# Optimization experiments

Hardware: AMD Instinct MI355X
Metric: run time of the kernel (lower is better)

Reference implementation:

```python
import jax, jax.numpy as jnp
import numpy as np

N_LAYERS = 2
N_COEF = 5
IN_DIM = 256
LN_EPS = 1e-6  # flax LayerNorm default


def jacobi_design(x, a, n):
    """Jacobi polynomials P_0..P_{n-1}^{(a,a)}(x). x: [...], returns [..., n]."""
    Ps = [jnp.ones_like(x)]
    if n > 1:
        Ps.append((a + 1.0) * x)
    for k in range(2, n):
        t = 2.0 * k + 2.0 * a
        A = 2.0 * k * (k + 2.0 * a) * (t - 2.0)
        B = (t - 1.0) * t * (t - 2.0)
        C = 2.0 * (k + a - 1.0) ** 2 * t
        Ps.append((B * x * Ps[-1] - C * Ps[-2]) / A)
    return jnp.stack(Ps, axis=-1)


def setup_inputs() -> dict:
    key = jax.random.key(0)
    k1, k2 = jax.random.split(key)
    x = jax.random.normal(k1, (8192, IN_DIM), dtype=jnp.float32)
    coefs = jax.random.normal(k2, (N_LAYERS, IN_DIM, IN_DIM, N_COEF), dtype=jnp.float32) * 0.03
    alphas = jnp.zeros((N_LAYERS,), dtype=jnp.float32)      # alpha_arctanh init zeros
    ln_scale = jnp.ones((N_LAYERS, IN_DIM), dtype=jnp.float32)
    ln_bias = jnp.zeros((N_LAYERS, IN_DIM), dtype=jnp.float32)
    return {"x": x, "coefs": coefs, "alphas": alphas, "ln_scale": ln_scale, "ln_bias": ln_bias}


def reference(x, coefs, alphas, ln_scale, ln_bias):
    h = x  # [B, D]
    for l in range(N_LAYERS):
        # LayerNorm
        mu = jnp.mean(h, axis=-1, keepdims=True)
        var = jnp.mean(jnp.square(h - mu), axis=-1, keepdims=True)
        hn = (h - mu) * jax.lax.rsqrt(var + LN_EPS) * ln_scale[l] + ln_bias[l]
        # KANLayer: Jacobi design matrix on tanh-mapped input
        a = jnp.tanh(alphas[l])
        dm = jacobi_design(jnp.tanh(hn), a, N_COEF)  # [B, D, C]
        # resid_scale=0, spline_scale=1, dropout inactive -> y = mean_i einsum
        in_dim = hn.shape[-1]
        h = jnp.einsum('bic,ioc->bo', dm, coefs[l]) / in_dim  # [B, D]
    return h
```

## Files before the change

### kernel.cpp

```cpp
#include <hip/hip_runtime.h>

#define D 256
#define NCOEF 5
#define KD 1280
#define NB 8192
#define NKC 160
#define PANEL (NKC * 512)

#define SXX_STRIDE 264
#define SXX_ELEMS (32 * SXX_STRIDE)

typedef __bf16 bf16;
typedef bf16 bf16x8 __attribute__((ext_vector_type(8)));
typedef bf16 bf16x4 __attribute__((ext_vector_type(4)));
typedef float f32x4 __attribute__((ext_vector_type(4)));

__device__ __forceinline__ void glds16(const bf16* g, bf16* l) {
    __builtin_amdgcn_global_load_lds((const __attribute__((address_space(1))) void*)g,
                                     (__attribute__((address_space(3))) void*)l, 16, 0, 0);
}

__global__ __launch_bounds__(256) void pack_kernel(const float* __restrict__ coefs,
                                                   bf16* __restrict__ Wt) {
    __shared__ float t[64 * 65];
    int b = blockIdx.x;
    int l = b / 80, rem = b % 80;
    int c = rem / 16, tl = rem % 16;
    int i0 = (tl >> 2) * 64, o0 = (tl & 3) * 64;

    for (int j = threadIdx.x; j < 4096; j += 256) {
        int i = j >> 6, o = j & 63;
        t[i * 65 + o] = coefs[(((size_t)(l * 256 + i0 + i)) * 256 + (o0 + o)) * 5 + c];
    }
    __syncthreads();
    bf16* dst = Wt + (size_t)l * (4 * PANEL)
                   + ((size_t)(tl & 3) * NKC + (c * 256 + i0) / 8) * 512;
    for (int j = threadIdx.x; j < 4096; j += 256) {
        int il = j & 7, o = (j >> 3) & 63, ih = j >> 9;
        dst[j] = (bf16)t[(ih * 8 + il) * 65 + o];
    }
}

template <int PH>
__device__ __forceinline__ void gemm_half(f32x4 (&acc)[2][4], const bf16* __restrict__ Wp,
                                          const bf16* sxx, bf16* sW, int l,
                                          float a1, const float* rB, const float* rC) {
#pragma unroll
    for (int it = 0; it < 20; ++it) {
        if (it == 19) __builtin_amdgcn_s_waitcnt(0x0F70);
        else          __builtin_amdgcn_s_waitcnt(0x0F74);
        const bf16* sWb = sW + (it & 1) * 2048;

        bf16x8 bfr[4];
#pragma unroll
        for (int tn = 0; tn < 4; ++tn)
            bfr[tn] = *(const bf16x8*)(sWb + (l >> 4) * 512 + (16 * tn + (l & 15)) * 8);

        const int kbase = PH * 640 + it * 32;
        const int c = kbase >> 8;
        const int i0 = (kbase & 255) + (l >> 4) * 8;

        bf16x8 af[2];
#pragma unroll
        for (int tm = 0; tm < 2; ++tm) {
            if (c == 0) {
#pragma unroll
                for (int j = 0; j < 8; ++j) af[tm][j] = (bf16)1.0f;
            } else {
                bf16x8 xv = *(const bf16x8*)(sxx + (16 * tm + (l & 15)) * SXX_STRIDE + i0);
#pragma unroll
                for (int j = 0; j < 8; ++j) {
                    float x = (float)xv[j];
                    float P;
                    if (c == 1)      P = a1 * x;
                    else if (c == 2) { float P1 = a1 * x; P = rB[0] * x * P1 - rC[0]; }
                    else if (c == 3) { float P1 = a1 * x; float P2 = rB[0] * x * P1 - rC[0];
                                       P = rB[1] * x * P2 - rC[1] * P1; }
                    else             { float P1 = a1 * x; float P2 = rB[0] * x * P1 - rC[0];
                                       float P3 = rB[1] * x * P2 - rC[1] * P1;
                                       P = rB[2] * x * P3 - rC[2] * P2; }
                    af[tm][j] = (bf16)P;
                }
            }
        }

#pragma unroll
        for (int tm = 0; tm < 2; ++tm)
#pragma unroll
            for (int tn = 0; tn < 4; ++tn)
                acc[tm][tn] = __builtin_amdgcn_mfma_f32_16x16x32_bf16(
                    af[tm], bfr[tn], acc[tm][tn], 0, 0, 0);

        if (it < 18) {
            __builtin_amdgcn_s_waitcnt(0xC07F);
            __builtin_amdgcn_sched_barrier(0);
            bf16* dst = sW + (it & 1) * 2048;
            const int kc0 = PH * 80 + (it + 2) * 4;
#pragma unroll
            for (int t = 0; t < 4; ++t)
                glds16(Wp + (kc0 + t) * 512 + l * 8, dst + t * 512);
        }
    }
}

__global__ __launch_bounds__(256, 2) void layer_kernel(
    const float* __restrict__ h, const float* __restrict__ scale,
    const float* __restrict__ bias, const float* __restrict__ alpha_p,
    const bf16* __restrict__ Wl, float* __restrict__ out) {
    __shared__ __align__(16) bf16 smem[SXX_ELEMS + 4 * 4096];

    const int tid = threadIdx.x;
    const int l   = tid & 63;
    const int w   = tid >> 6;
    const int g   = w >> 1, p = w & 1;
    const int slab = blockIdx.x >> 1;
    const int ch   = blockIdx.x & 1;

    bf16* sxx = smem;
    bf16* sW  = smem + SXX_ELEMS + w * 4096;

    const float a  = tanhf(alpha_p[0]);
    const float a1 = a + 1.f;
    float rB[3], rC[3];
#pragma unroll
    for (int k = 2; k < NCOEF; k++) {
        float tk  = 2.f * k + 2.f * a;
        float iAk = 1.f / (2.f * k * (k + 2.f * a) * (tk - 2.f));
        rB[k - 2] = (tk - 1.f) * tk * (tk - 2.f) * iAk;
        rC[k - 2] = 2.f * (k + a - 1.f) * (k + a - 1.f) * tk * iAk;
    }

    float4 sc4 = ((const float4*)scale)[l];
    float4 bi4 = ((const float4*)bias)[l];
    float scv[4] = {sc4.x, sc4.y, sc4.z, sc4.w};
    float biv[4] = {bi4.x, bi4.y, bi4.z, bi4.w};

    const float* hrows = h + (size_t)slab * 32 * D;
#pragma unroll
    for (int rr = 0; rr < 8; ++rr) {
        int lr = w * 8 + rr;
        float4 v = ((const float4*)(hrows + lr * D))[l];
        float s  = v.x + v.y + v.z + v.w;
        float ss = v.x * v.x + v.y * v.y + v.z * v.z + v.w * v.w;
#pragma unroll
        for (int off = 32; off > 0; off >>= 1) {
            s  += __shfl_down(s, off);
            ss += __shfl_down(ss, off);
        }
        s  = __shfl(s, 0);
        ss = __shfl(ss, 0);
        float mu   = s * (1.f / D);
        float rstd = rsqrtf(ss * (1.f / D) - mu * mu + 1e-6f);
        float hv[4] = {v.x, v.y, v.z, v.w};
        bf16x4 o;
#pragma unroll
        for (int e = 0; e < 4; ++e)
            o[e] = (bf16)tanhf((hv[e] - mu) * rstd * scv[e] + biv[e]);
        *(bf16x4*)(sxx + lr * SXX_STRIDE + 4 * l) = o;
    }

    const bf16* Wp = Wl + (size_t)(ch * 2 + g) * PANEL;
#pragma unroll
    for (int it = 0; it < 2; ++it) {
        bf16* dst = sW + it * 2048;
        const int kc0 = p * 80 + it * 4;
#pragma unroll
        for (int t = 0; t < 4; ++t)
            glds16(Wp + (kc0 + t) * 512 + l * 8, dst + t * 512);
    }
    __syncthreads();

    f32x4 acc[2][4] = {};
    if (p == 0) gemm_half<0>(acc, Wp, sxx, sW, l, a1, rB, rC);
    else        gemm_half<1>(acc, Wp, sxx, sW, l, a1, rB, rC);

    f32x4* dump = (f32x4*)(smem + SXX_ELEMS) + w * 512;
#pragma unroll
    for (int tm = 0; tm < 2; ++tm)
#pragma unroll
        for (int tn = 0; tn < 4; ++tn)
            dump[(tm * 4 + tn) * 64 + l] = acc[tm][tn];
    __syncthreads();

    if (p == 0) {
        f32x4* mine = dump;
        f32x4* part = dump + 512;
#pragma unroll
        for (int tm = 0; tm < 2; ++tm)
#pragma unroll
            for (int tn = 0; tn < 4; ++tn) {
                f32x4 v = mine[(tm * 4 + tn) * 64 + l] + part[(tm * 4 + tn) * 64 + l];
                v *= (1.f / 256.f);
                int gr = slab * 32 + 16 * tm + (l >> 4) * 4;
                int gc = ch * 128 + g * 64 + 16 * tn + (l & 15);
#pragma unroll
                for (int r = 0; r < 4; ++r)
                    out[(size_t)(gr + r) * D + gc] = v[r];
            }
    }
}

extern "C" void kernel_launch(void* const* d_in, const int* in_sizes, int n_in,
                              void* d_out, int out_size, void* d_ws, size_t ws_size,
                              hipStream_t stream) {
    const float* x        = (const float*)d_in[0];
    const float* coefs    = (const float*)d_in[1];
    const float* alphas   = (const float*)d_in[2];
    const float* ln_scale = (const float*)d_in[3];
    const float* ln_bias  = (const float*)d_in[4];
    float* out = (float*)d_out;

    char* ws = (char*)d_ws;
    bf16*  Wt = (bf16*)ws;
    float* h1 = (float*)(ws + 1310720);

    pack_kernel<<<160, 256, 0, stream>>>(coefs, Wt);
    layer_kernel<<<512, 256, 0, stream>>>(x, ln_scale, ln_bias, alphas, Wt, h1);
    layer_kernel<<<512, 256, 0, stream>>>(h1, ln_scale + D, ln_bias + D, alphas + 1,
                                          Wt + (size_t)4 * PANEL, out);
}
```

Baseline: 110.1 us.

## Fold constant P0 term into per-output bias and shrink GEMM K to 1024

The P0 Jacobi term is constant 1, so its contribution becomes a precomputed per-output bias (the column sum of coefs[...,0]), computed in extra pack_kernel blocks and added in the epilogue. This cuts GEMM K from 1280 to 1024. The remaining planes are reordered so each wave's pair of K-steps shares one evaluation of the polynomial recurrence, with the second operand cached in registers. tanhf is replaced by an exp-based fast tanh, which has slightly different accuracy near zero.

```diff
diff --git a/kernel.cpp b/kernel.cpp
--- a/kernel.cpp
+++ b/kernel.cpp
@@ -1,10 +1,9 @@
 #include <hip/hip_runtime.h>
 
 #define D 256
-#define NCOEF 5
-#define KD 1280
 #define NB 8192
-#define NKC 160
+#define KP 1024
+#define NKC 128
 #define PANEL (NKC * 512)
 
 #define SXX_STRIDE 264
@@ -20,34 +19,60 @@
                                      (__attribute__((address_space(3))) void*)l, 16, 0, 0);
 }
 
+__device__ __forceinline__ float fast_tanh(float x) {
+    float e = __expf(2.f * x);
+    return 1.f - 2.f / (e + 1.f);
+}
+
 __global__ __launch_bounds__(256) void pack_kernel(const float* __restrict__ coefs,
-                                                   bf16* __restrict__ Wt) {
+                                                   bf16* __restrict__ Wt,
+                                                   float* __restrict__ beta) {
     __shared__ float t[64 * 65];
+    __shared__ float accs[4][64];
     int b = blockIdx.x;
-    int l = b / 80, rem = b % 80;
-    int c = rem / 16, tl = rem % 16;
-    int i0 = (tl >> 2) * 64, o0 = (tl & 3) * 64;
-
-    for (int j = threadIdx.x; j < 4096; j += 256) {
-        int i = j >> 6, o = j & 63;
-        t[i * 65 + o] = coefs[(((size_t)(l * 256 + i0 + i)) * 256 + (o0 + o)) * 5 + c];
-    }
-    __syncthreads();
-    bf16* dst = Wt + (size_t)l * (4 * PANEL)
-                   + ((size_t)(tl & 3) * NKC + (c * 256 + i0) / 8) * 512;
-    for (int j = threadIdx.x; j < 4096; j += 256) {
-        int il = j & 7, o = (j >> 3) & 63, ih = j >> 9;
-        dst[j] = (bf16)t[(ih * 8 + il) * 65 + o];
+    if (b < 128) {
+        int l = b >> 6, rem = b & 63;
+        int c = (rem >> 4) + 1, tl = rem & 15;
+        int plane = (c == 1) ? 0 : (c == 4) ? 1 : (c == 2) ? 2 : 3;
+        int i0 = (tl >> 2) * 64, o0 = (tl & 3) * 64;
+
+        for (int j = threadIdx.x; j < 4096; j += 256) {
+            int i = j >> 6, o = j & 63;
+            t[i * 65 + o] = coefs[(((size_t)(l * 256 + i0 + i)) * 256 + (o0 + o)) * 5 + c];
+        }
+        __syncthreads();
+        bf16* dst = Wt + (size_t)l * (4 * PANEL)
+                       + ((size_t)(tl & 3) * NKC + (plane * 256 + i0) / 8) * 512;
+        for (int j = threadIdx.x; j < 4096; j += 256) {
+            int il = j & 7, o = (j >> 3) & 63, ih = j >> 9;
+            dst[j] = (bf16)t[(ih * 8 + il) * 65 + o];
+        }
+    } else {
+        int lidx = b - 128;
+        int l = lidx >> 2, o0 = (lidx & 3) * 64;
+        int o = threadIdx.x & 63, ig = threadIdx.x >> 6;
+        float sum = 0.f;
+        for (int m = 0; m < 64; ++m) {
+            int i = ig * 64 + m;
+            sum += coefs[(((size_t)(l * 256 + i)) * 256 + (o0 + o)) * 5 + 0];
+        }
+        accs[ig][o] = sum;
+        __syncthreads();
+        if (threadIdx.x < 64)
+            beta[l * 256 + o0 + threadIdx.x] = accs[0][threadIdx.x] + accs[1][threadIdx.x]
+                                             + accs[2][threadIdx.x] + accs[3][threadIdx.x];
     }
 }
 
 template <int PH>
 __device__ __forceinline__ void gemm_half(f32x4 (&acc)[2][4], const bf16* __restrict__ Wp,
-                                          const bf16* sxx, bf16* sW, int l,
-                                          float a1, const float* rB, const float* rC) {
-#pragma unroll
-    for (int it = 0; it < 20; ++it) {
-        if (it == 19) __builtin_amdgcn_s_waitcnt(0x0F70);
+                                          const bf16* sxx, bf16* sW, int l, float a1,
+                                          float rB0, float rB1, float rB2,
+                                          float rC0, float rC1, float rC2) {
+    bf16x8 afn[2];
+#pragma unroll
+    for (int it = 0; it < 16; ++it) {
+        if (it == 15) __builtin_amdgcn_s_waitcnt(0x0F70);
         else          __builtin_amdgcn_s_waitcnt(0x0F74);
         const bf16* sWb = sW + (it & 1) * 2048;
 
@@ -56,32 +81,29 @@
         for (int tn = 0; tn < 4; ++tn)
             bfr[tn] = *(const bf16x8*)(sWb + (l >> 4) * 512 + (16 * tn + (l & 15)) * 8);
 
-        const int kbase = PH * 640 + it * 32;
-        const int c = kbase >> 8;
-        const int i0 = (kbase & 255) + (l >> 4) * 8;
-
         bf16x8 af[2];
-#pragma unroll
-        for (int tm = 0; tm < 2; ++tm) {
-            if (c == 0) {
-#pragma unroll
-                for (int j = 0; j < 8; ++j) af[tm][j] = (bf16)1.0f;
-            } else {
+        if ((it & 1) == 0) {
+            const int j  = it >> 1;
+            const int i0 = j * 32 + (l >> 4) * 8;
+#pragma unroll
+            for (int tm = 0; tm < 2; ++tm) {
                 bf16x8 xv = *(const bf16x8*)(sxx + (16 * tm + (l & 15)) * SXX_STRIDE + i0);
 #pragma unroll
-                for (int j = 0; j < 8; ++j) {
-                    float x = (float)xv[j];
-                    float P;
-                    if (c == 1)      P = a1 * x;
-                    else if (c == 2) { float P1 = a1 * x; P = rB[0] * x * P1 - rC[0]; }
-                    else if (c == 3) { float P1 = a1 * x; float P2 = rB[0] * x * P1 - rC[0];
-                                       P = rB[1] * x * P2 - rC[1] * P1; }
-                    else             { float P1 = a1 * x; float P2 = rB[0] * x * P1 - rC[0];
-                                       float P3 = rB[1] * x * P2 - rC[1] * P1;
-                                       P = rB[2] * x * P3 - rC[2] * P2; }
-                    af[tm][j] = (bf16)P;
+                for (int jj = 0; jj < 8; ++jj) {
+                    float x  = (float)xv[jj];
+                    float P1 = a1 * x;
+                    float P2 = rB0 * x * P1 - rC0;
+                    float P3 = rB1 * x * P2 - rC1 * P1;
+                    float PA, PB;
+                    if (PH == 0) { PA = P1; PB = rB2 * x * P3 - rC2 * P2; }
+                    else         { PA = P2; PB = P3; }
+                    af[tm][jj]  = (bf16)PA;
+                    afn[tm][jj] = (bf16)PB;
                 }
             }
+        } else {
+            af[0] = afn[0];
+            af[1] = afn[1];
         }
 
 #pragma unroll
@@ -91,14 +113,15 @@
                 acc[tm][tn] = __builtin_amdgcn_mfma_f32_16x16x32_bf16(
                     af[tm], bfr[tn], acc[tm][tn], 0, 0, 0);
 
-        if (it < 18) {
+        if (it < 14) {
             __builtin_amdgcn_s_waitcnt(0xC07F);
             __builtin_amdgcn_sched_barrier(0);
+            const int itp   = it + 2;
+            const int chunk = (PH * 2 + (itp & 1)) * 8 + (itp >> 1);
             bf16* dst = sW + (it & 1) * 2048;
-            const int kc0 = PH * 80 + (it + 2) * 4;
 #pragma unroll
             for (int t = 0; t < 4; ++t)
-                glds16(Wp + (kc0 + t) * 512 + l * 8, dst + t * 512);
+                glds16(Wp + chunk * 2048 + t * 512 + l * 8, dst + t * 512);
         }
     }
 }
@@ -106,7 +129,8 @@
 __global__ __launch_bounds__(256, 2) void layer_kernel(
     const float* __restrict__ h, const float* __restrict__ scale,
     const float* __restrict__ bias, const float* __restrict__ alpha_p,
-    const bf16* __restrict__ Wl, float* __restrict__ out) {
+    const bf16* __restrict__ Wl, const float* __restrict__ beta,
+    float* __restrict__ out) {
     __shared__ __align__(16) bf16 smem[SXX_ELEMS + 4 * 4096];
 
     const int tid = threadIdx.x;
@@ -123,7 +147,7 @@
     const float a1 = a + 1.f;
     float rB[3], rC[3];
 #pragma unroll
-    for (int k = 2; k < NCOEF; k++) {
+    for (int k = 2; k < 5; k++) {
         float tk  = 2.f * k + 2.f * a;
         float iAk = 1.f / (2.f * k * (k + 2.f * a) * (tk - 2.f));
         rB[k - 2] = (tk - 1.f) * tk * (tk - 2.f) * iAk;
@@ -155,24 +179,24 @@
         bf16x4 o;
 #pragma unroll
         for (int e = 0; e < 4; ++e)
-            o[e] = (bf16)tanhf((hv[e] - mu) * rstd * scv[e] + biv[e]);
+            o[e] = (bf16)fast_tanh((hv[e] - mu) * rstd * scv[e] + biv[e]);
         *(bf16x4*)(sxx + lr * SXX_STRIDE + 4 * l) = o;
     }
 
     const bf16* Wp = Wl + (size_t)(ch * 2 + g) * PANEL;
 #pragma unroll
-    for (int it = 0; it < 2; ++it) {
-        bf16* dst = sW + it * 2048;
-        const int kc0 = p * 80 + it * 4;
+    for (int itp = 0; itp < 2; ++itp) {
+        bf16* dst = sW + itp * 2048;
+        const int chunk = (p * 2 + itp) * 8;
 #pragma unroll
         for (int t = 0; t < 4; ++t)
-            glds16(Wp + (kc0 + t) * 512 + l * 8, dst + t * 512);
+            glds16(Wp + chunk * 2048 + t * 512 + l * 8, dst + t * 512);
     }
     __syncthreads();
 
     f32x4 acc[2][4] = {};
-    if (p == 0) gemm_half<0>(acc, Wp, sxx, sW, l, a1, rB, rC);
-    else        gemm_half<1>(acc, Wp, sxx, sW, l, a1, rB, rC);
+    if (p == 0) gemm_half<0>(acc, Wp, sxx, sW, l, a1, rB[0], rB[1], rB[2], rC[0], rC[1], rC[2]);
+    else        gemm_half<1>(acc, Wp, sxx, sW, l, a1, rB[0], rB[1], rB[2], rC[0], rC[1], rC[2]);
 
     f32x4* dump = (f32x4*)(smem + SXX_ELEMS) + w * 512;
 #pragma unroll
@@ -189,13 +213,13 @@
         for (int tm = 0; tm < 2; ++tm)
 #pragma unroll
             for (int tn = 0; tn < 4; ++tn) {
+                int gc = ch * 128 + g * 64 + 16 * tn + (l & 15);
+                float bv = beta[gc] * (1.f / 256.f);
                 f32x4 v = mine[(tm * 4 + tn) * 64 + l] + part[(tm * 4 + tn) * 64 + l];
-                v *= (1.f / 256.f);
                 int gr = slab * 32 + 16 * tm + (l >> 4) * 4;
-                int gc = ch * 128 + g * 64 + 16 * tn + (l & 15);
 #pragma unroll
                 for (int r = 0; r < 4; ++r)
-                    out[(size_t)(gr + r) * D + gc] = v[r];
+                    out[(size_t)(gr + r) * D + gc] = v[r] * (1.f / 256.f) + bv;
             }
     }
 }
@@ -211,11 +235,12 @@
     float* out = (float*)d_out;
 
     char* ws = (char*)d_ws;
-    bf16*  Wt = (bf16*)ws;
-    float* h1 = (float*)(ws + 1310720);
-
-    pack_kernel<<<160, 256, 0, stream>>>(coefs, Wt);
-    layer_kernel<<<512, 256, 0, stream>>>(x, ln_scale, ln_bias, alphas, Wt, h1);
+    bf16*  Wt   = (bf16*)ws;
+    float* beta = (float*)(ws + 1048576);
+    float* h1   = (float*)(ws + 1048576 + 2048);
+
+    pack_kernel<<<136, 256, 0, stream>>>(coefs, Wt, beta);
+    layer_kernel<<<512, 256, 0, stream>>>(x, ln_scale, ln_bias, alphas, Wt, beta, h1);
     layer_kernel<<<512, 256, 0, stream>>>(h1, ln_scale + D, ln_bias + D, alphas + 1,
-                                          Wt + (size_t)4 * PANEL, out);
-}
+                                          Wt + (size_t)4 * PANEL, beta + D, out);
+}
```

Result: faster. 103.8 us (-5.7%).
